# Optimization experiments

Measured on AMD Instinct MI355X. Metric: run time of the kernel, lower is better.

The kernel has to match this reference:

```python
import jax, jax.numpy as jnp
import numpy as np

D_IN = 1024
D_OUT = 1024
NUM_HEADS = 16
HEAD_DIM = D_OUT // NUM_HEADS


def setup_inputs() -> dict:
    key = jax.random.key(0)
    k = jax.random.split(key, 6)
    s = 1.0 / np.sqrt(D_IN)
    return {
        "x": jax.random.normal(k[0], (2, 2048, D_IN), dtype=jnp.float32),
        "W_q": jax.random.uniform(k[1], (D_OUT, D_IN), jnp.float32, -s, s),
        "W_k": jax.random.uniform(k[2], (D_OUT, D_IN), jnp.float32, -s, s),
        "W_v": jax.random.uniform(k[3], (D_OUT, D_IN), jnp.float32, -s, s),
        "W_o": jax.random.uniform(k[4], (D_OUT, D_OUT), jnp.float32, -s, s),
        "b_o": jax.random.uniform(k[5], (D_OUT,), jnp.float32, -s, s),
    }


def reference(x, W_q, W_k, W_v, W_o, b_o):
    b, n, _ = x.shape
    h, hd = NUM_HEADS, HEAD_DIM
    # linear projections (torch Linear: x @ W.T), reshape to [b, h, n, hd]
    q = (x @ W_q.T).reshape(b, n, h, hd).transpose(0, 2, 1, 3)
    k = (x @ W_k.T).reshape(b, n, h, hd).transpose(0, 2, 1, 3)
    v = (x @ W_v.T).reshape(b, n, h, hd).transpose(0, 2, 1, 3)
    scores = jnp.einsum("bhqd,bhkd->bhqk", q, k) / np.sqrt(hd).astype(np.float32)
    causal = jnp.triu(jnp.full((n, n), -jnp.inf, dtype=scores.dtype), k=1)
    scores = scores + causal[None, None]
    weights = jax.nn.softmax(scores, axis=-1)  # dropout p=0.0 -> identity
    ctx = jnp.einsum("bhqk,bhkd->bhqd", weights, v)
    ctx = ctx.transpose(0, 2, 1, 3).reshape(b, n, h * hd)
    return ctx @ W_o.T + b_o
```

## Files before the change

### kernel.cpp

```cpp
#include <hip/hip_runtime.h>
#include <hip/hip_bf16.h>
#include <stdint.h>

typedef __attribute__((ext_vector_type(8)))  __bf16   bf16x8;
typedef __attribute__((ext_vector_type(4)))  float    f32x4;
typedef __attribute__((ext_vector_type(16))) float    f32x16;
typedef __attribute__((ext_vector_type(4)))  unsigned u32x4;
typedef __attribute__((ext_vector_type(2)))  unsigned u32x2;

#define BATCH  2
#define SEQ    2048
#define DMODEL 1024
#define NHEAD  16
#define HDIM   64
#define MTOT   (BATCH * SEQ)
#define MOFF   8.0f

__device__ __forceinline__ void gload_lds16(const void* g, void* l) {
  __builtin_amdgcn_global_load_lds(
      (const __attribute__((address_space(1))) unsigned int*)g,
      (__attribute__((address_space(3))) unsigned int*)(uintptr_t)l,
      16, 0, 0);
}

__device__ __forceinline__ unsigned pkbf(float a, float b) {
  unsigned lo = (unsigned)__builtin_bit_cast(unsigned short, (__bf16)a);
  unsigned hb = (unsigned)__builtin_bit_cast(unsigned short, (__bf16)b);
  return lo | (hb << 16);
}

__global__ void cast_all(const float* __restrict__ x,  const float* __restrict__ wq,
                         const float* __restrict__ wk, const float* __restrict__ wv,
                         const float* __restrict__ wo,
                         __bf16* __restrict__ xb,  __bf16* __restrict__ wqb,
                         __bf16* __restrict__ wkb, __bf16* __restrict__ wvb,
                         __bf16* __restrict__ wob)
{
  const float* in; __bf16* out; int n;
  switch (blockIdx.y) {
    case 0:  in = x;  out = xb;  n = MTOT * DMODEL;   break;
    case 1:  in = wq; out = wqb; n = DMODEL * DMODEL; break;
    case 2:  in = wk; out = wkb; n = DMODEL * DMODEL; break;
    case 3:  in = wv; out = wvb; n = DMODEL * DMODEL; break;
    default: in = wo; out = wob; n = DMODEL * DMODEL; break;
  }
  const int i = blockIdx.x * blockDim.x + threadIdx.x;
  const int stride = gridDim.x * blockDim.x;
  for (int idx = i; idx * 8 < n; idx += stride) {
    const float4 a = ((const float4*)in)[idx * 2];
    const float4 b = ((const float4*)in)[idx * 2 + 1];
    bf16x8 v = { (__bf16)a.x, (__bf16)a.y, (__bf16)a.z, (__bf16)a.w,
                 (__bf16)b.x, (__bf16)b.y, (__bf16)b.z, (__bf16)b.w };
    *(bf16x8*)(out + (size_t)idx * 8) = v;
  }
}

__device__ __forceinline__ void gemm_tile_128(const __bf16* __restrict__ A,
                                              const __bf16* __restrict__ W,
                                              int bm, int bn, int Kd,
                                              f32x4 (&acc)[4][4])
{
  __shared__ __align__(16) __bf16 As[128 * 32];
  __shared__ __align__(16) __bf16 Bs[128 * 32];
  const int tid  = threadIdx.x;
  const int wave = tid >> 6, lane = tid & 63;
  const int wr = wave >> 1, wc = wave & 1;
  const int fr = lane & 15, fq = lane >> 4;
  const int c0 = tid, c1 = tid + 256;
  const __bf16* gA0 = A + (size_t)(bm * 128 + (c0 >> 2)) * Kd + (c0 & 3) * 8;
  const __bf16* gA1 = A + (size_t)(bm * 128 + (c1 >> 2)) * Kd + (c1 & 3) * 8;
  const __bf16* gB0 = W + (size_t)(bn * 128 + (c0 >> 2)) * Kd + (c0 & 3) * 8;
  const __bf16* gB1 = W + (size_t)(bn * 128 + (c1 >> 2)) * Kd + (c1 & 3) * 8;

  for (int k0 = 0; k0 < Kd; k0 += 32) {
    gload_lds16(gA0 + k0, As + c0 * 8);
    gload_lds16(gB0 + k0, Bs + c0 * 8);
    gload_lds16(gA1 + k0, As + c1 * 8);
    gload_lds16(gB1 + k0, Bs + c1 * 8);
    __syncthreads();
    bf16x8 a[4], b[4];
#pragma unroll
    for (int m = 0; m < 4; ++m)
      a[m] = *(const bf16x8*)(As + (wr * 64 + m * 16 + fr) * 32 + fq * 8);
#pragma unroll
    for (int n = 0; n < 4; ++n)
      b[n] = *(const bf16x8*)(Bs + (wc * 64 + n * 16 + fr) * 32 + fq * 8);
#pragma unroll
    for (int m = 0; m < 4; ++m)
#pragma unroll
      for (int n = 0; n < 4; ++n)
        acc[m][n] = __builtin_amdgcn_mfma_f32_16x16x32_bf16(a[m], b[n], acc[m][n], 0, 0, 0);
    __syncthreads();
  }
}

__global__ __launch_bounds__(256)
void gemm_qkv(const __bf16* __restrict__ xb,
              const __bf16* __restrict__ Wq, const __bf16* __restrict__ Wk,
              const __bf16* __restrict__ Wv,
              __bf16* __restrict__ Qo, __bf16* __restrict__ Ko, __bf16* __restrict__ VTo,
              float qscale)
{
  const int z = blockIdx.z;
  const __bf16* A; const __bf16* W; __bf16* Ob; int bm, bn;
  if (z == 2)      { A = Wv; W = xb; Ob = VTo; bm = blockIdx.y; bn = blockIdx.x; }
  else if (z == 1) { A = xb; W = Wk; Ob = Ko;  bm = blockIdx.x; bn = blockIdx.y; }
  else             { A = xb; W = Wq; Ob = Qo;  bm = blockIdx.x; bn = blockIdx.y; }

  f32x4 acc[4][4] = {};
  gemm_tile_128(A, W, bm, bn, DMODEL, acc);

  const int lane = threadIdx.x & 63, wave = threadIdx.x >> 6;
  const int wr = wave >> 1, wc = wave & 1;
  const int fr = lane & 15, fq = lane >> 4;

  if (z == 0) {
#pragma unroll
    for (int m = 0; m < 4; ++m)
#pragma unroll
      for (int n = 0; n < 4; ++n) {
        const int col = bn * 128 + wc * 64 + n * 16 + fr;
#pragma unroll
        for (int j = 0; j < 4; ++j) {
          const int row = bm * 128 + wr * 64 + m * 16 + fq * 4 + j;
          Ob[(size_t)row * DMODEL + col] = (__bf16)(acc[m][n][j] * qscale);
        }
      }
  } else if (z == 1) {
#pragma unroll
    for (int m = 0; m < 4; ++m)
#pragma unroll
      for (int n = 0; n < 4; ++n) {
        const int f = bn * 128 + wc * 64 + n * 16 + fr;
        const int h = f >> 6;
        const int kc = (f >> 4) & 3, hi = (f >> 3) & 1, jj = f & 7;
#pragma unroll
        for (int j = 0; j < 4; ++j) {
          const int tkn = bm * 128 + wr * 64 + m * 16 + fq * 4 + j;
          const int bb = tkn >> 11, n2 = tkn & 2047;
          const int t32 = n2 >> 5, ln2 = n2 & 31;
          const size_t idx = (((((size_t)bb * 16 + h) * 64 + t32) * 4 + kc) * 64
                              + (ln2 + (hi << 5))) * 8 + jj;
          Ob[idx] = (__bf16)acc[m][n][j];
        }
      }
  } else {
#pragma unroll
    for (int m = 0; m < 4; ++m)
#pragma unroll
      for (int n = 0; n < 4; ++n) {
        const int tkn = bn * 128 + wc * 64 + n * 16 + fr;
        const int bb = tkn >> 11, n2 = tkn & 2047;
        const int t64 = n2 >> 6, w2 = n2 & 63;
        const int kc = w2 >> 4, hi = (w2 >> 3) & 1, jj = w2 & 7;
#pragma unroll
        for (int j = 0; j < 4; ++j) {
          const int f = bm * 128 + wr * 64 + m * 16 + fq * 4 + j;
          const int h = f >> 6, d = f & 63;
          const int db = d >> 5, ln2 = d & 31;
          const size_t idx = ((((((size_t)bb * 16 + h) * 32 + t64) * 2 + db) * 4 + kc) * 64
                              + (ln2 + (hi << 5))) * 8 + jj;
          Ob[idx] = (__bf16)acc[m][n][j];
        }
      }
  }
}

__global__ __launch_bounds__(512)
void gemm_out(const __bf16* __restrict__ A, const __bf16* __restrict__ W,
              float* __restrict__ OF, const float* __restrict__ bias)
{
  __shared__ __align__(16) __bf16 As[2][128 * 32];
  __shared__ __align__(16) __bf16 Bs[2][128 * 32];
  __shared__ __align__(16) float  Cred[4 * 16 * 64 * 4];

  const int tid  = threadIdx.x;
  const int wave = tid >> 6, lane = tid & 63;
  const int g    = wave >> 2;
  const int w4   = wave & 3;
  const int wr = w4 >> 1, wc = w4 & 1;
  const int fr = lane & 15, fq = lane >> 4;
  const int bm = blockIdx.x, bn = blockIdx.y;

  const int tid2 = tid & 255;
  const int c0 = tid2, c1 = tid2 + 256;
  const int kgo = g * 512;
  const __bf16* gA0 = A + (size_t)(bm * 128 + (c0 >> 2)) * DMODEL + (c0 & 3) * 8 + kgo;
  const __bf16* gA1 = A + (size_t)(bm * 128 + (c1 >> 2)) * DMODEL + (c1 & 3) * 8 + kgo;
  const __bf16* gB0 = W + (size_t)(bn * 128 + (c0 >> 2)) * DMODEL + (c0 & 3) * 8 + kgo;
  const __bf16* gB1 = W + (size_t)(bn * 128 + (c1 >> 2)) * DMODEL + (c1 & 3) * 8 + kgo;
  __bf16* Asg = As[g];
  __bf16* Bsg = Bs[g];

  f32x4 acc[4][4] = {};

  for (int k0 = 0; k0 < 512; k0 += 32) {
    gload_lds16(gA0 + k0, Asg + c0 * 8);
    gload_lds16(gB0 + k0, Bsg + c0 * 8);
    gload_lds16(gA1 + k0, Asg + c1 * 8);
    gload_lds16(gB1 + k0, Bsg + c1 * 8);
    __syncthreads();
    bf16x8 a[4], b[4];
#pragma unroll
    for (int m = 0; m < 4; ++m)
      a[m] = *(const bf16x8*)(Asg + (wr * 64 + m * 16 + fr) * 32 + fq * 8);
#pragma unroll
    for (int n = 0; n < 4; ++n)
      b[n] = *(const bf16x8*)(Bsg + (wc * 64 + n * 16 + fr) * 32 + fq * 8);
#pragma unroll
    for (int m = 0; m < 4; ++m)
#pragma unroll
      for (int n = 0; n < 4; ++n)
        acc[m][n] = __builtin_amdgcn_mfma_f32_16x16x32_bf16(a[m], b[n], acc[m][n], 0, 0, 0);
    __syncthreads();
  }

  if (g == 1) {
#pragma unroll
    for (int m = 0; m < 4; ++m)
#pragma unroll
      for (int n = 0; n < 4; ++n)
        *(f32x4*)&Cred[(((w4 * 16) + m * 4 + n) * 64 + lane) * 4] = acc[m][n];
  }
  __syncthreads();

  if (g == 0) {
#pragma unroll
    for (int m = 0; m < 4; ++m)
#pragma unroll
      for (int n = 0; n < 4; ++n) {
        const f32x4 part = *(const f32x4*)&Cred[(((w4 * 16) + m * 4 + n) * 64 + lane) * 4];
        const int col = bn * 128 + wc * 64 + n * 16 + fr;
        const float bv = bias[col];
#pragma unroll
        for (int j = 0; j < 4; ++j) {
          const int row = bm * 128 + wr * 64 + m * 16 + fq * 4 + j;
          OF[(size_t)row * DMODEL + col] = acc[m][n][j] + part[j] + bv;
        }
      }
  }
}


__device__ __forceinline__ void mask_tile(f32x16& sv0, f32x16& sv1,
                                          int kv0, int q0, int ln, int hi)
{
  const int qg = q0 + ln;
#pragma unroll
  for (int r = 0; r < 16; ++r) {
    const int kvo = kv0 + (r & 3) + 8 * (r >> 2) + 4 * hi;
    if (kvo > qg)      sv0[r] = -1e30f;
    if (kvo + 32 > qg) sv1[r] = -1e30f;
  }
}

__device__ __forceinline__ void pack_pf(const f32x16& sv0, const f32x16& sv1,
                                        bf16x8 (&pf)[4], int hi)
{
#pragma unroll
  for (int half = 0; half < 2; ++half) {
    const int r0 = half * 8;
    {
      unsigned pk01 = pkbf(sv0[r0 + 0], sv0[r0 + 1]);
      unsigned pk23 = pkbf(sv0[r0 + 2], sv0[r0 + 3]);
      unsigned pk45 = pkbf(sv0[r0 + 4], sv0[r0 + 5]);
      unsigned pk67 = pkbf(sv0[r0 + 6], sv0[r0 + 7]);
      unsigned x01 = (unsigned)__shfl_xor((int)pk01, 32, 64);
      unsigned x23 = (unsigned)__shfl_xor((int)pk23, 32, 64);
      unsigned x45 = (unsigned)__shfl_xor((int)pk45, 32, 64);
      unsigned x67 = (unsigned)__shfl_xor((int)pk67, 32, 64);
      u32x4 uw = { hi ? x45 : pk01, hi ? x67 : pk23,
                   hi ? pk45 : x01, hi ? pk67 : x23 };
      pf[half] = __builtin_bit_cast(bf16x8, uw);
    }
    {
      unsigned pk01 = pkbf(sv1[r0 + 0], sv1[r0 + 1]);
      unsigned pk23 = pkbf(sv1[r0 + 2], sv1[r0 + 3]);
      unsigned pk45 = pkbf(sv1[r0 + 4], sv1[r0 + 5]);
      unsigned pk67 = pkbf(sv1[r0 + 6], sv1[r0 + 7]);
      unsigned x01 = (unsigned)__shfl_xor((int)pk01, 32, 64);
      unsigned x23 = (unsigned)__shfl_xor((int)pk23, 32, 64);
      unsigned x45 = (unsigned)__shfl_xor((int)pk45, 32, 64);
      unsigned x67 = (unsigned)__shfl_xor((int)pk67, 32, 64);
      u32x4 uw = { hi ? x45 : pk01, hi ? x67 : pk23,
                   hi ? pk45 : x01, hi ? pk67 : x23 };
      pf[2 + half] = __builtin_bit_cast(bf16x8, uw);
    }
  }
}

__global__ __launch_bounds__(128, 3)
void attn_kernel(const __bf16* __restrict__ Qg, const __bf16* __restrict__ PK,
                 const __bf16* __restrict__ PV, __bf16* __restrict__ Og)
{
  __shared__ __align__(16) float Cs[2][32][68];
  __shared__ float Ls[2][2][32];

  const int tid  = threadIdx.x;
  const int p    = tid >> 6;
  const int lane = tid & 63;
  const int ln = lane & 31, hi = lane >> 5;
  const int bI = blockIdx.x;
  const int bh = bI & 31;
  const int qt = 63 - (bI >> 5);
  const int b = bh >> 4, h = bh & 15;

  const int q0 = qt * 32;
  const int nt = (qt >> 1) + 1;

  const __bf16* Kp = PK + (size_t)(b * 16 + h) * (64 * 4 * 64 * 8);
  const __bf16* Vp = PV + (size_t)(b * 16 + h) * (32 * 2 * 4 * 64 * 8);
  const __bf16* Qp = Qg + ((size_t)b * SEQ + q0 + ln) * DMODEL + h * HDIM + hi * 8;

  bf16x8 qf[4];
#pragma unroll
  for (int kc = 0; kc < 4; ++kc)
    qf[kc] = *(const bf16x8*)(Qp + kc * 16);

  f32x16 c0 = {}, c1 = {};
  float l = 0.f;

  for (int t = p; t < nt; t += 2) {
    const __bf16* kt = Kp + (size_t)t * 4096;
    const __bf16* vt = Vp + (size_t)t * 4096;

    bf16x8 kA[4], kB[4];
#pragma unroll
    for (int kc = 0; kc < 4; ++kc) {
      kA[kc] = *(const bf16x8*)(kt + (kc * 64 + lane) * 8);
      kB[kc] = *(const bf16x8*)(kt + 2048 + (kc * 64 + lane) * 8);
    }

    f32x16 s0 = {}, s1 = {};
    __builtin_amdgcn_s_setprio(1);
#pragma unroll
    for (int kc = 0; kc < 4; ++kc) {
      s0 = __builtin_amdgcn_mfma_f32_32x32x16_bf16(kA[kc], qf[kc], s0, 0, 0, 0);
      s1 = __builtin_amdgcn_mfma_f32_32x32x16_bf16(kB[kc], qf[kc], s1, 0, 0, 0);
    }
    __builtin_amdgcn_s_setprio(0);

    bf16x8 vt0[4], vt1[4];
#pragma unroll
    for (int kc = 0; kc < 4; ++kc) {
      vt0[kc] = *(const bf16x8*)(vt + (kc * 64 + lane) * 8);
      vt1[kc] = *(const bf16x8*)(vt + 2048 + (kc * 64 + lane) * 8);
    }

    if (t == nt - 1) mask_tile(s0, s1, t * 64, q0, ln, hi);

#pragma unroll
    for (int r = 0; r < 16; ++r) {
      s0[r] = __builtin_amdgcn_exp2f(s0[r] - MOFF);
      s1[r] = __builtin_amdgcn_exp2f(s1[r] - MOFF);
    }
    float s8[8];
#pragma unroll
    for (int r = 0; r < 8; ++r)
      s8[r] = (s0[r] + s0[r + 8]) + (s1[r] + s1[r + 8]);
#pragma unroll
    for (int r = 0; r < 4; ++r) s8[r] += s8[r + 4];
    l += (s8[0] + s8[1]) + (s8[2] + s8[3]);

    bf16x8 pf[4];
    pack_pf(s0, s1, pf, hi);

    __builtin_amdgcn_s_setprio(1);
#pragma unroll
    for (int kc = 0; kc < 4; ++kc)
      c0 = __builtin_amdgcn_mfma_f32_32x32x16_bf16(vt0[kc], pf[kc], c0, 0, 0, 0);
#pragma unroll
    for (int kc = 0; kc < 4; ++kc)
      c1 = __builtin_amdgcn_mfma_f32_32x32x16_bf16(vt1[kc], pf[kc], c1, 0, 0, 0);
    __builtin_amdgcn_s_setprio(0);
  }

#pragma unroll
  for (int g = 0; g < 4; ++g) {
    f32x4 v0 = { c0[4*g+0], c0[4*g+1], c0[4*g+2], c0[4*g+3] };
    f32x4 v1 = { c1[4*g+0], c1[4*g+1], c1[4*g+2], c1[4*g+3] };
    *(f32x4*)&Cs[p][ln][g * 8 + hi * 4]      = v0;
    *(f32x4*)&Cs[p][ln][32 + g * 8 + hi * 4] = v1;
  }
  Ls[p][hi][ln] = l;
  __syncthreads();

  const int qe = p * 16 + (lane >> 2);
  const int de = (lane & 3) * 16;
  const float lt = Ls[0][0][qe] + Ls[0][1][qe] + Ls[1][0][qe] + Ls[1][1][qe];
  const float inv = 1.0f / lt;
  f32x4 a0 = *(const f32x4*)&Cs[0][qe][de]      + *(const f32x4*)&Cs[1][qe][de];
  f32x4 a1 = *(const f32x4*)&Cs[0][qe][de + 4]  + *(const f32x4*)&Cs[1][qe][de + 4];
  f32x4 a2 = *(const f32x4*)&Cs[0][qe][de + 8]  + *(const f32x4*)&Cs[1][qe][de + 8];
  f32x4 a3 = *(const f32x4*)&Cs[0][qe][de + 12] + *(const f32x4*)&Cs[1][qe][de + 12];
  u32x4 w0 = { pkbf(a0[0] * inv, a0[1] * inv), pkbf(a0[2] * inv, a0[3] * inv),
               pkbf(a1[0] * inv, a1[1] * inv), pkbf(a1[2] * inv, a1[3] * inv) };
  u32x4 w1 = { pkbf(a2[0] * inv, a2[1] * inv), pkbf(a2[2] * inv, a2[3] * inv),
               pkbf(a3[0] * inv, a3[1] * inv), pkbf(a3[2] * inv, a3[3] * inv) };
  __bf16* Op = Og + ((size_t)b * SEQ + q0 + qe) * DMODEL + h * HDIM + de;
  *(u32x4*)(Op)     = w0;
  *(u32x4*)(Op + 8) = w1;
}

extern "C" void kernel_launch(void* const* d_in, const int* in_sizes, int n_in,
                              void* d_out, int out_size, void* d_ws, size_t ws_size,
                              hipStream_t stream) {
  (void)in_sizes; (void)n_in; (void)out_size; (void)ws_size;
  const float* x  = (const float*)d_in[0];
  const float* Wq = (const float*)d_in[1];
  const float* Wk = (const float*)d_in[2];
  const float* Wv = (const float*)d_in[3];
  const float* Wo = (const float*)d_in[4];
  const float* bo = (const float*)d_in[5];
  float* out = (float*)d_out;

  __bf16* ws  = (__bf16*)d_ws;
  __bf16* xb  = ws;
  __bf16* Wqb = xb  + (size_t)MTOT * DMODEL;
  __bf16* Wkb = Wqb + (size_t)DMODEL * DMODEL;
  __bf16* Wvb = Wkb + (size_t)DMODEL * DMODEL;
  __bf16* Wob = Wvb + (size_t)DMODEL * DMODEL;
  __bf16* Qb  = Wob + (size_t)DMODEL * DMODEL;
  __bf16* Kpk = Qb  + (size_t)MTOT * DMODEL;
  __bf16* Vpk = Kpk + (size_t)MTOT * DMODEL;
  __bf16* ctxb = xb;

  cast_all<<<dim3(256, 5), 256, 0, stream>>>(x, Wq, Wk, Wv, Wo,
                                             xb, Wqb, Wkb, Wvb, Wob);

  const float qscale = 0.125f * 1.4426950408889634f;
  gemm_qkv<<<dim3(32, 8, 3), 256, 0, stream>>>(xb, Wqb, Wkb, Wvb, Qb, Kpk, Vpk, qscale);

  attn_kernel<<<dim3(2048), 128, 0, stream>>>(Qb, Kpk, Vpk, ctxb);

  gemm_out<<<dim3(32, 8), 512, 0, stream>>>(ctxb, Wob, out, bo);
}
```

Baseline: 98.25 us.

## Double-buffer K/V tile loads in registers to prefetch next tile

```diff
diff --git a/kernel.cpp b/kernel.cpp
--- a/kernel.cpp
+++ b/kernel.cpp
@@ -289,7 +289,61 @@
   }
 }
 
-__global__ __launch_bounds__(128, 3)
+__device__ __forceinline__ void attn_step(
+    const __bf16* __restrict__ Kp, const __bf16* __restrict__ Vp, int tn,
+    bf16x8 (&kAc)[4], bf16x8 (&kBc)[4], bf16x8 (&v0c)[4], bf16x8 (&v1c)[4],
+    bf16x8 (&kAn)[4], bf16x8 (&kBn)[4], bf16x8 (&v0n)[4], bf16x8 (&v1n)[4],
+    const bf16x8 (&qf)[4], f32x16& c0, f32x16& c1, float& l,
+    bool domask, int t, int q0, int ln, int hi, int lane)
+{
+  f32x16 s0 = {}, s1 = {};
+  __builtin_amdgcn_s_setprio(1);
+#pragma unroll
+  for (int kc = 0; kc < 4; ++kc) {
+    s0 = __builtin_amdgcn_mfma_f32_32x32x16_bf16(kAc[kc], qf[kc], s0, 0, 0, 0);
+    s1 = __builtin_amdgcn_mfma_f32_32x32x16_bf16(kBc[kc], qf[kc], s1, 0, 0, 0);
+  }
+  __builtin_amdgcn_s_setprio(0);
+
+  const __bf16* ktn = Kp + (size_t)tn * 4096;
+  const __bf16* vtn = Vp + (size_t)tn * 4096;
+#pragma unroll
+  for (int kc = 0; kc < 4; ++kc) {
+    kAn[kc] = *(const bf16x8*)(ktn + (kc * 64 + lane) * 8);
+    kBn[kc] = *(const bf16x8*)(ktn + 2048 + (kc * 64 + lane) * 8);
+    v0n[kc] = *(const bf16x8*)(vtn + (kc * 64 + lane) * 8);
+    v1n[kc] = *(const bf16x8*)(vtn + 2048 + (kc * 64 + lane) * 8);
+  }
+
+  if (domask) mask_tile(s0, s1, t * 64, q0, ln, hi);
+
+#pragma unroll
+  for (int r = 0; r < 16; ++r) {
+    s0[r] = __builtin_amdgcn_exp2f(s0[r] - MOFF);
+    s1[r] = __builtin_amdgcn_exp2f(s1[r] - MOFF);
+  }
+  float s8[8];
+#pragma unroll
+  for (int r = 0; r < 8; ++r)
+    s8[r] = (s0[r] + s0[r + 8]) + (s1[r] + s1[r + 8]);
+#pragma unroll
+  for (int r = 0; r < 4; ++r) s8[r] += s8[r + 4];
+  l += (s8[0] + s8[1]) + (s8[2] + s8[3]);
+
+  bf16x8 pf[4];
+  pack_pf(s0, s1, pf, hi);
+
+  __builtin_amdgcn_s_setprio(1);
+#pragma unroll
+  for (int kc = 0; kc < 4; ++kc)
+    c0 = __builtin_amdgcn_mfma_f32_32x32x16_bf16(v0c[kc], pf[kc], c0, 0, 0, 0);
+#pragma unroll
+  for (int kc = 0; kc < 4; ++kc)
+    c1 = __builtin_amdgcn_mfma_f32_32x32x16_bf16(v1c[kc], pf[kc], c1, 0, 0, 0);
+  __builtin_amdgcn_s_setprio(0);
+}
+
+__global__ __launch_bounds__(128, 2)
 void attn_kernel(const __bf16* __restrict__ Qg, const __bf16* __restrict__ PK,
                  const __bf16* __restrict__ PV, __bf16* __restrict__ Og)
 {
@@ -307,6 +361,7 @@
 
   const int q0 = qt * 32;
   const int nt = (qt >> 1) + 1;
+  const int tcl = nt - 1;
 
   const __bf16* Kp = PK + (size_t)(b * 16 + h) * (64 * 4 * 64 * 8);
   const __bf16* Vp = PV + (size_t)(b * 16 + h) * (32 * 2 * 4 * 64 * 8);
@@ -320,59 +375,41 @@
   f32x16 c0 = {}, c1 = {};
   float l = 0.f;
 
-  for (int t = p; t < nt; t += 2) {
-    const __bf16* kt = Kp + (size_t)t * 4096;
-    const __bf16* vt = Vp + (size_t)t * 4096;
-
-    bf16x8 kA[4], kB[4];
+  bf16x8 kA_A[4], kB_A[4], v0_A[4], v1_A[4];
+  bf16x8 kA_B[4], kB_B[4], v0_B[4], v1_B[4];
+
+  {
+    const int t0 = (p <= tcl) ? p : tcl;
+    const __bf16* kt = Kp + (size_t)t0 * 4096;
+    const __bf16* vt = Vp + (size_t)t0 * 4096;
 #pragma unroll
     for (int kc = 0; kc < 4; ++kc) {
-      kA[kc] = *(const bf16x8*)(kt + (kc * 64 + lane) * 8);
-      kB[kc] = *(const bf16x8*)(kt + 2048 + (kc * 64 + lane) * 8);
+      kA_A[kc] = *(const bf16x8*)(kt + (kc * 64 + lane) * 8);
+      kB_A[kc] = *(const bf16x8*)(kt + 2048 + (kc * 64 + lane) * 8);
+      v0_A[kc] = *(const bf16x8*)(vt + (kc * 64 + lane) * 8);
+      v1_A[kc] = *(const bf16x8*)(vt + 2048 + (kc * 64 + lane) * 8);
     }
-
-    f32x16 s0 = {}, s1 = {};
-    __builtin_amdgcn_s_setprio(1);
-#pragma unroll
-    for (int kc = 0; kc < 4; ++kc) {
-      s0 = __builtin_amdgcn_mfma_f32_32x32x16_bf16(kA[kc], qf[kc], s0, 0, 0, 0);
-      s1 = __builtin_amdgcn_mfma_f32_32x32x16_bf16(kB[kc], qf[kc], s1, 0, 0, 0);
+  }
+
+  int t = p;
+  while (t < nt) {
+    {
+      const int tn = (t + 2 <= tcl) ? t + 2 : tcl;
+      attn_step(Kp, Vp, tn,
+                kA_A, kB_A, v0_A, v1_A,
+                kA_B, kB_B, v0_B, v1_B,
+                qf, c0, c1, l, t == nt - 1, t, q0, ln, hi, lane);
     }
-    __builtin_amdgcn_s_setprio(0);
-
-    bf16x8 vt0[4], vt1[4];
-#pragma unroll
-    for (int kc = 0; kc < 4; ++kc) {
-      vt0[kc] = *(const bf16x8*)(vt + (kc * 64 + lane) * 8);
-      vt1[kc] = *(const bf16x8*)(vt + 2048 + (kc * 64 + lane) * 8);
+    t += 2;
+    if (t >= nt) break;
+    {
+      const int tn = (t + 2 <= tcl) ? t + 2 : tcl;
+      attn_step(Kp, Vp, tn,
+                kA_B, kB_B, v0_B, v1_B,
+                kA_A, kB_A, v0_A, v1_A,
+                qf, c0, c1, l, t == nt - 1, t, q0, ln, hi, lane);
     }
-
-    if (t == nt - 1) mask_tile(s0, s1, t * 64, q0, ln, hi);
-
-#pragma unroll
-    for (int r = 0; r < 16; ++r) {
-      s0[r] = __builtin_amdgcn_exp2f(s0[r] - MOFF);
-      s1[r] = __builtin_amdgcn_exp2f(s1[r] - MOFF);
-    }
-    float s8[8];
-#pragma unroll
-    for (int r = 0; r < 8; ++r)
-      s8[r] = (s0[r] + s0[r + 8]) + (s1[r] + s1[r + 8]);
-#pragma unroll
-    for (int r = 0; r < 4; ++r) s8[r] += s8[r + 4];
-    l += (s8[0] + s8[1]) + (s8[2] + s8[3]);
-
-    bf16x8 pf[4];
-    pack_pf(s0, s1, pf, hi);
-
-    __builtin_amdgcn_s_setprio(1);
-#pragma unroll
-    for (int kc = 0; kc < 4; ++kc)
-      c0 = __builtin_amdgcn_mfma_f32_32x32x16_bf16(vt0[kc], pf[kc], c0, 0, 0, 0);
-#pragma unroll
-    for (int kc = 0; kc < 4; ++kc)
-      c1 = __builtin_amdgcn_mfma_f32_32x32x16_bf16(vt1[kc], pf[kc], c1, 0, 0, 0);
-    __builtin_amdgcn_s_setprio(0);
+    t += 2;
   }
 
 #pragma unroll
```

New measurement: 101.9 us. +3.7%, slower.
